# Performance work log

Measured on AMD Instinct MI355X. Metric: run time of the kernel, lower is better.

The kernel has to match this reference:

```python
import jax, jax.numpy as jnp
import numpy as np

V = 32000   # vocab_size
E = 512     # embedding_dim
H = 512     # hidden_dim
B = 16      # batch
T = 128     # max_decoder_length
S = 512     # max_encoder_length
D = 2       # directions (bidirectional encoder)


def setup_inputs() -> dict:
    key = jax.random.key(0)
    ks = jax.random.split(key, 16)
    sc = 0.02
    x = jax.random.randint(ks[0], (B, T), 0, V, dtype=jnp.int32)
    x_lengths = jax.random.randint(ks[1], (B,), 1, T + 1, dtype=jnp.int32)
    h0 = jax.random.normal(ks[2], (1, B, H), jnp.float32) * sc
    c0 = jax.random.normal(ks[3], (1, B, H), jnp.float32) * sc
    encoder_outputs = jax.random.normal(ks[4], (B, S, D * H), jnp.float32) * sc
    emb = jax.random.normal(ks[5], (V, E), jnp.float32) * sc
    emb = emb.at[0].set(0.0)  # padding_idx=0
    W_att = jax.random.normal(ks[6], (2 * H + E, S), jnp.float32) * sc
    b_att = jnp.zeros((S,), jnp.float32)
    W_ih = jax.random.normal(ks[7], (4 * H, E + H), jnp.float32) * sc
    W_hh = jax.random.normal(ks[8], (4 * H, H), jnp.float32) * sc
    b_ih = jnp.zeros((4 * H,), jnp.float32)
    b_hh = jnp.zeros((4 * H,), jnp.float32)
    W_align = jax.random.normal(ks[9], (2 * H, H), jnp.float32) * sc
    b_align = jnp.zeros((H,), jnp.float32)
    W_out = jax.random.normal(ks[10], (H, V), jnp.float32) * sc
    b_out = jnp.zeros((V,), jnp.float32)
    return dict(x=x, x_lengths=x_lengths, h0=h0, c0=c0,
                encoder_outputs=encoder_outputs, emb=emb,
                W_att=W_att, b_att=b_att,
                W_ih=W_ih, W_hh=W_hh, b_ih=b_ih, b_hh=b_hh,
                W_align=W_align, b_align=b_align,
                W_out=W_out, b_out=b_out)


def reference(x, x_lengths, h0, c0, encoder_outputs, emb, W_att, b_att,
              W_ih, W_hh, b_ih, b_hh, W_align, b_align, W_out, b_out):
    # embedding (dropout_rate=0 -> identity)
    xe = emb[x]                                       # [B,T,E]
    # context from initial state (num_layers=1)
    context = (h0 + c0).reshape(B, 1, H)              # view(B, L, H), L=1
    context = jnp.sum(context, axis=1, keepdims=True) # [B,1,H]
    context = jnp.broadcast_to(context, (B, T, H))
    lstm_input = jnp.concatenate([context, xe], axis=-1)  # [B,T,H+E]

    # single-layer LSTM over time with packed-sequence semantics:
    # state frozen and output zeroed for t >= length
    def step(carry, inp):
        h, c = carry
        x_t, t = inp                                   # x_t: [B,H+E]
        gates = x_t @ W_ih.T + h @ W_hh.T + b_ih + b_hh
        i, f, g, o = jnp.split(gates, 4, axis=-1)
        i = jax.nn.sigmoid(i); f = jax.nn.sigmoid(f)
        g = jnp.tanh(g);       o = jax.nn.sigmoid(o)
        c_new = f * c + i * g
        h_new = o * jnp.tanh(c_new)
        valid = (t < x_lengths)[:, None]
        h2 = jnp.where(valid, h_new, h)
        c2 = jnp.where(valid, c_new, c)
        return (h2, c2), jnp.where(valid, h_new, 0.0)

    ts = jnp.arange(T)
    (_, _), outs = jax.lax.scan(step, (h0[0], c0[0]),
                                (jnp.swapaxes(lstm_input, 0, 1), ts))
    lstm_output = jnp.swapaxes(outs, 0, 1)            # [B,T,H]

    # encoder_outputs: view(dir, B, S, H) then sum over directions
    enc = encoder_outputs.reshape(D, B, S, H).sum(0)  # [B,S,H]

    attention_input = jnp.concatenate([lstm_output, lstm_input], axis=-1)  # [B,T,2H+E]
    att_logits = jax.lax.stop_gradient(attention_input @ W_att + b_att)    # no_grad in torch
    soft = jax.nn.softmax(att_logits, axis=-1)        # [B,T,S]
    h_t_bar = jnp.einsum('bts,bsh->bth', soft, enc)   # [B,T,H]

    # attention targets: 0 at t=0, (S//T)*t otherwise
    tgt_row = (S // T) * jnp.arange(T, dtype=jnp.int32)
    tgt_row = tgt_row.at[0].set(0)
    attention_targets = jnp.broadcast_to(tgt_row, (B, T))

    aligned = jax.nn.sigmoid(
        jnp.concatenate([lstm_output, h_t_bar], axis=-1) @ W_align + b_align)
    out = lstm_output + h_t_bar * aligned
    out = out @ W_out + b_out                          # [B,T,V]
    return (out, jax.lax.stop_gradient(attention_input), attention_targets)
```

## Files before the change

kernel.cpp:

```cpp
#include <hip/hip_runtime.h>
#include <hip/hip_bf16.h>
#include <math.h>


typedef __attribute__((ext_vector_type(8))) short short8;
typedef __attribute__((ext_vector_type(4))) float floatx4;
typedef __attribute__((ext_vector_type(4))) int intx4;
typedef __hip_bfloat16 bf16;

__device__ __forceinline__ float b2f(bf16 v){ return __bfloat162float(v); }
__device__ __forceinline__ bf16 f2b(float v){ return __float2bfloat16(v); }
__device__ __forceinline__ float ld(const void* p, long i, int f32){
  return f32 ? ((const float*)p)[i] : b2f(((const bf16*)p)[i]);
}

__global__ void k_detect(const unsigned short* __restrict__ h0u, int* __restrict__ flags){
  if (threadIdx.x == 0){
    int bad = 0;
    for (int i=0;i<256;i++){
      int e = (h0u[i] >> 7) & 0xFF;
      if (e != 0 && (e < 100 || e > 140)) bad++;
    }
    flags[0] = (bad > 32) ? 1 : 0;
    flags[1] = 0;
  }
}

__global__ void k_prep(const int* __restrict__ x, const void* __restrict__ h0,
                       const void* __restrict__ c0, const void* __restrict__ emb,
                       const int* __restrict__ flags, bf16* __restrict__ lstm_input,
                       bf16* __restrict__ att_ws, float* __restrict__ state0,
                       bf16* __restrict__ hbuf){
  int f32 = flags[0];
  int idx = blockIdx.x*256 + threadIdx.x;
  int m = idx >> 10, c = idx & 1023;
  float v;
  if (c < 512){
    int b = m >> 7;
    v = ld(h0, b*512 + c, f32) + ld(c0, b*512 + c, f32);
  } else {
    v = ld(emb, (long)x[m]*512 + (c - 512), f32);
  }
  bf16 bv = f2b(v);
  lstm_input[idx] = bv;
  att_ws[(long)m*1536 + 512 + c] = bv;
  if (idx < 8192){
    float hv = ld(h0, idx, f32), cv = ld(c0, idx, f32);
    hbuf[idx] = f2b(hv);
    state0[idx] = hv;
    state0[8192 + idx] = cv;
  }
}

__global__ void k_encT(const void* __restrict__ eo, const int* __restrict__ flags,
                       bf16* __restrict__ encT){
  __shared__ float tile[32][33];
  int f32 = flags[0];
  int b = blockIdx.z;
  int s0 = blockIdx.x*32, h0 = blockIdx.y*32;
  int tx = threadIdx.x, ty = threadIdx.y;
  #pragma unroll
  for (int j=0;j<4;j++){
    int s = s0 + ty + j*8;
    long o = (long)b*262144 + (long)s*512 + h0 + tx;
    tile[ty + j*8][tx] = ld(eo, o, f32) + ld(eo, 4194304 + o, f32);
  }
  __syncthreads();
  #pragma unroll
  for (int j=0;j<4;j++){
    int h = h0 + ty + j*8;
    encT[((long)b*512 + h)*512 + s0 + tx] = f2b(tile[tx][ty + j*8]);
  }
}

__global__ void k_tr(const void* __restrict__ in, bf16* __restrict__ out,
                     int R, int C, const int* __restrict__ flags){
  __shared__ float tile[32][33];
  int f32 = flags[0];
  int c0 = blockIdx.x*32, r0 = blockIdx.y*32;
  int tx = threadIdx.x, ty = threadIdx.y;
  #pragma unroll
  for (int j=0;j<4;j++)
    tile[ty+j*8][tx] = ld(in, (long)(r0+ty+j*8)*C + c0+tx, f32);
  __syncthreads();
  #pragma unroll
  for (int j=0;j<4;j++)
    out[(long)(c0+ty+j*8)*R + r0+tx] = f2b(tile[tx][ty+j*8]);
}

__global__ void k_cvtW(const void* __restrict__ w, const int* __restrict__ flags,
                       bf16* __restrict__ out, long n){
  int f32 = flags[0];
  long i = (long)blockIdx.x*256 + threadIdx.x;
  if (i < n) out[i] = f2b(ld(w, i, f32));
}

__global__ void k_cvt(const void* bih, const void* bhh, const void* batt,
                      const void* balign, const void* bout,
                      const int* __restrict__ flags, bf16* __restrict__ bb){
  int f32 = flags[0];
  int i = blockIdx.x*256 + threadIdx.x;
  if (i < 2048)      bb[i] = f2b(ld(bih, i, f32));
  else if (i < 4096) bb[i] = f2b(ld(bhh, i-2048, f32));
  else if (i < 4608) bb[i] = f2b(ld(batt, i-4096, f32));
  else if (i < 5120) bb[i] = f2b(ld(balign, i-4608, f32));
  else if (i < 37120) bb[i] = f2b(ld(bout, i-5120, f32));
}

__global__ void k_wswz(const void* __restrict__ whh, const int* __restrict__ flags,
                       bf16* __restrict__ wsw){
  int f32 = flags[0];
  int bid = blockIdx.x;
  int l = threadIdx.x;
  int p = bid >> 7, tt = (bid >> 4) & 7, ks = bid & 15;
  int g = tt >> 1, hh = tt & 1;
  int row = g*512 + p*32 + hh*16 + (l & 15);
  int k = ks*32 + (l >> 4)*8;
  #pragma unroll
  for (int j=0;j<8;j++)
    wsw[(long)(bid*64 + l)*8 + j] = f2b(ld(whh, (long)row*512 + k + j, f32));
}

#define M_GX    0
#define M_F32   1
#define M_BF16  2
#define M_ALIGN 3
#define M_OUT   4

template<int MODE>
__global__ void __launch_bounds__(256)
k_gemm(const bf16* __restrict__ A, const bf16* __restrict__ Bm, int K,
       float* __restrict__ outF, bf16* __restrict__ outBH, void* __restrict__ outO,
       int ldc, const bf16* __restrict__ bias1, const bf16* __restrict__ bias2,
       const bf16* __restrict__ alin, bf16* __restrict__ finin,
       const int* __restrict__ flags, long aZ, long bZ, long cZ){
  __shared__ __align__(16) bf16 As[128*32];
  __shared__ __align__(16) bf16 Bs[128*32];
  int dfl = 0;
  if constexpr (MODE == M_OUT) dfl = flags[0];
  int tid = threadIdx.x;
  int w = tid >> 6, l = tid & 63;
  int bm = blockIdx.x, bn = blockIdx.y, bz = blockIdx.z;
  const bf16* Ag = A + bz*aZ + (long)(bm*128 + (tid>>2))*K + (tid&3)*8;
  const bf16* Bg = Bm + bz*bZ + (long)(bn*128 + (tid>>2))*K + (tid&3)*8;
  int m0 = (w&1)*64, n0 = (w>>1)*64;
  floatx4 acc[4][4];
  #pragma unroll
  for (int i=0;i<4;i++)
    #pragma unroll
    for (int j=0;j<4;j++){ floatx4 z = {0.f,0.f,0.f,0.f}; acc[i][j] = z; }

  for (int k0=0; k0<K; k0+=32){
    short8 a0 = *(const short8*)(Ag + k0);
    short8 a1 = *(const short8*)(Ag + (long)64*K + k0);
    short8 b0 = *(const short8*)(Bg + k0);
    short8 b1 = *(const short8*)(Bg + (long)64*K + k0);
    __syncthreads();
    *(short8*)(As + tid*8)        = a0;
    *(short8*)(As + 2048 + tid*8) = a1;
    *(short8*)(Bs + tid*8)        = b0;
    *(short8*)(Bs + 2048 + tid*8) = b1;
    __syncthreads();
    short8 af[4], bfr[4];
    #pragma unroll
    for (int i=0;i<4;i++){
      af[i]  = *(const short8*)(As + (m0 + i*16 + (l&15))*32 + (l>>4)*8);
      bfr[i] = *(const short8*)(Bs + (n0 + i*16 + (l&15))*32 + (l>>4)*8);
    }
    #pragma unroll
    for (int i=0;i<4;i++)
      #pragma unroll
      for (int j=0;j<4;j++)
        acc[i][j] = __builtin_amdgcn_mfma_f32_16x16x32_bf16(af[i], bfr[j], acc[i][j], 0,0,0);
  }

  int rbase = (l>>4)*4;
  int cl = l & 15;
  #pragma unroll
  for (int i=0;i<4;i++){
    #pragma unroll
    for (int j=0;j<4;j++){
      int col = bn*128 + n0 + j*16 + cl;
      #pragma unroll
      for (int r=0;r<4;r++){
        int row = bm*128 + m0 + i*16 + rbase + r;
        float v = acc[i][j][r];
        if constexpr (MODE == M_GX){
          v += b2f(bias1[col]) + b2f(bias2[col]);
          int t = row & 127, b = row >> 7;
          outF[(long)(t*16 + b)*2048 + col] = v;
        } else if constexpr (MODE == M_F32){
          v += b2f(bias1[col]);
          outF[(long)row*ldc + col] = v;
        } else if constexpr (MODE == M_BF16){
          outBH[bz*cZ + (long)row*ldc + col] = f2b(v);
        } else if constexpr (MODE == M_ALIGN){
          v += b2f(bias1[col]);
          float sg = 1.0f/(1.0f + __expf(-v));
          float lo = b2f(alin[(long)row*1024 + col]);
          float hb = b2f(alin[(long)row*1024 + 512 + col]);
          finin[(long)row*512 + col] = f2b(lo + hb*sg);
        } else {
          v += b2f(bias1[col]);
          if (dfl) ((float*)outO)[(long)row*ldc + col] = v;
          else     ((bf16*)outO)[(long)row*ldc + col] = f2b(v);
        }
      }
    }
  }
}

__global__ void k_softmax(const float* __restrict__ lg, bf16* __restrict__ soft){
  __shared__ float red[256];
  int r = blockIdx.x;
  int tid = threadIdx.x;
  float x0 = lg[(long)r*512 + tid], x1 = lg[(long)r*512 + 256 + tid];
  red[tid] = fmaxf(x0, x1); __syncthreads();
  for (int s=128; s>0; s>>=1){ if (tid<s) red[tid] = fmaxf(red[tid], red[tid+s]); __syncthreads(); }
  float mx = red[0]; __syncthreads();
  float e0 = __expf(x0-mx), e1 = __expf(x1-mx);
  red[tid] = e0+e1; __syncthreads();
  for (int s=128; s>0; s>>=1){ if (tid<s) red[tid] += red[tid+s]; __syncthreads(); }
  float inv = 1.0f/red[0];
  soft[(long)r*512 + tid] = f2b(e0*inv);
  soft[(long)r*512 + 256 + tid] = f2b(e1*inv);
}

__global__ void __launch_bounds__(256, 1)
k_lstm(const float* __restrict__ gxT, const bf16* __restrict__ wsw,
       const int* __restrict__ xlen, const float* __restrict__ state0,
       bf16* __restrict__ hbuf, int* __restrict__ flags,
       bf16* __restrict__ att_ws, bf16* __restrict__ align_in){
  int* bar = flags + 1;
  int p = blockIdx.x;
  int tid = threadIdx.x;
  int w = tid >> 6, l = tid & 63;
  __shared__ float gx_sh[16*128];
  __shared__ __align__(16) bf16 hsh[16*32];
  __shared__ int lens[16];
  if (tid < 16) lens[tid] = xlen[tid];

  short8 wfrag[2][16];
  #pragma unroll
  for (int hh=0; hh<2; hh++)
    #pragma unroll
    for (int ks=0; ks<16; ks++)
      wfrag[hh][ks] = ((const short8*)wsw)[((p*8 + (w*2+hh))*16 + ks)*64 + l];

  int b0i = tid >> 5, u = tid & 31;
  int b1i = b0i + 8;
  float h_r0 = state0[b0i*512 + p*32 + u];
  float c_r0 = state0[8192 + b0i*512 + p*32 + u];
  float h_r1 = state0[b1i*512 + p*32 + u];
  float c_r1 = state0[8192 + b1i*512 + p*32 + u];

  float gr[8];
  #pragma unroll
  for (int rep=0;rep<8;rep++){
    int idx = rep*256 + tid;
    int b = idx >> 7, jl = idx & 127;
    gr[rep] = gxT[(long)b*2048 + (jl>>5)*512 + p*32 + (jl&31)];
  }

  __syncthreads();

  for (int t=0; t<128; t++){
    #pragma unroll
    for (int rep=0;rep<8;rep++)
      gx_sh[rep*256 + tid] = gr[rep];
    if (t < 127){
      #pragma unroll
      for (int rep=0;rep<8;rep++){
        int idx = rep*256 + tid;
        int b = idx >> 7, jl = idx & 127;
        gr[rep] = gxT[(long)((t+1)*16 + b)*2048 + (jl>>5)*512 + p*32 + (jl&31)];
      }
    }
    const bf16* hb = hbuf + (long)t*8192;
    floatx4 acc0 = {0.f,0.f,0.f,0.f};
    floatx4 acc1 = {0.f,0.f,0.f,0.f};
    #pragma unroll
    for (int ks=0; ks<16; ks++){
      short8 afr = *(const short8*)(hb + (l&15)*512 + ks*32 + (l>>4)*8);
      acc0 = __builtin_amdgcn_mfma_f32_16x16x32_bf16(afr, wfrag[0][ks], acc0, 0,0,0);
      acc1 = __builtin_amdgcn_mfma_f32_16x16x32_bf16(afr, wfrag[1][ks], acc1, 0,0,0);
    }
    __syncthreads();
    #pragma unroll
    for (int r=0; r<4; r++){
      int bb = (l>>4)*4 + r;
      gx_sh[bb*128 + w*32 + (l&15)]      += acc0[r];
      gx_sh[bb*128 + w*32 + 16 + (l&15)] += acc1[r];
    }
    __syncthreads();
    {
      float ig = gx_sh[b0i*128 + u],      fg = gx_sh[b0i*128 + 32 + u];
      float gg = gx_sh[b0i*128 + 64 + u], og = gx_sh[b0i*128 + 96 + u];
      bool valid = (t < lens[b0i]);
      float ii = 1.f/(1.f+__expf(-ig)), ff = 1.f/(1.f+__expf(-fg));
      float g2 = tanhf(gg),             oo = 1.f/(1.f+__expf(-og));
      float cn = ff*c_r0 + ii*g2;
      float hn = oo*tanhf(cn);
      if (valid){ c_r0 = cn; h_r0 = hn; }
      float hout = valid ? hn : 0.0f;
      hsh[b0i*32 + u] = f2b(h_r0);
      int row = b0i*128 + t;
      att_ws[(long)row*1536 + p*32 + u]   = f2b(hout);
      align_in[(long)row*1024 + p*32 + u] = f2b(hout);
    }
    {
      float ig = gx_sh[b1i*128 + u],      fg = gx_sh[b1i*128 + 32 + u];
      float gg = gx_sh[b1i*128 + 64 + u], og = gx_sh[b1i*128 + 96 + u];
      bool valid = (t < lens[b1i]);
      float ii = 1.f/(1.f+__expf(-ig)), ff = 1.f/(1.f+__expf(-fg));
      float g2 = tanhf(gg),             oo = 1.f/(1.f+__expf(-og));
      float cn = ff*c_r1 + ii*g2;
      float hn = oo*tanhf(cn);
      if (valid){ c_r1 = cn; h_r1 = hn; }
      float hout = valid ? hn : 0.0f;
      hsh[b1i*32 + u] = f2b(h_r1);
      int row = b1i*128 + t;
      att_ws[(long)row*1536 + p*32 + u]   = f2b(hout);
      align_in[(long)row*1024 + p*32 + u] = f2b(hout);
    }
    __syncthreads();
    if (t < 127){
      if (tid < 64){
        int b = tid >> 2, ch = tid & 3;
        intx4 hv = *(const intx4*)(hsh + b*32 + ch*8);
        bf16* dst = hbuf + (long)(t+1)*8192 + b*512 + p*32 + ch*8;
        asm volatile("global_store_dwordx4 %0, %1, off sc0 sc1" :: "v"(dst), "v"(hv) : "memory");
        asm volatile("s_waitcnt vmcnt(0)" ::: "memory");
        if (tid == 0){
          __hip_atomic_fetch_add(bar, 1, __ATOMIC_RELAXED, __HIP_MEMORY_SCOPE_AGENT);
          int target = (t+1)*16;
          while (__hip_atomic_load(bar, __ATOMIC_RELAXED, __HIP_MEMORY_SCOPE_AGENT) < target)
            __builtin_amdgcn_s_sleep(1);
        }
      }
      __syncthreads();
      asm volatile("" ::: "memory");
    }
  }
}

__global__ void k_finout(const bf16* __restrict__ att_ws, const int* __restrict__ flags,
                         void* __restrict__ d_out){
  int f32 = flags[0];
  long i = (long)blockIdx.x*256 + threadIdx.x;
  if (i < 3145728){
    if (f32) ((float*)d_out)[65536000 + i] = b2f(att_ws[i]);
    else     ((bf16*)d_out)[65536000 + i] = att_ws[i];
  } else if (i < 3147776){
    long j = i - 3145728;
    float tv = (float)(4*((int)j & 127));
    if (f32) ((float*)d_out)[68681728 + j] = tv;
    else     ((bf16*)d_out)[68681728 + j] = f2b(tv);
  }
}

extern "C" void kernel_launch(void* const* d_in, const int* in_sizes, int n_in,
                              void* d_out, int out_size, void* d_ws, size_t ws_size,
                              hipStream_t stream){
  const int*  x      = (const int*) d_in[0];
  const int*  xlen   = (const int*) d_in[1];
  const void* h0     = d_in[2];
  const void* c0     = d_in[3];
  const void* eo     = d_in[4];
  const void* emb    = d_in[5];
  const void* W_att  = d_in[6];
  const void* b_att  = d_in[7];
  const void* W_ih   = d_in[8];
  const void* W_hh   = d_in[9];
  const void* b_ih   = d_in[10];
  const void* b_hh   = d_in[11];
  const void* W_align= d_in[12];
  const void* b_align= d_in[13];
  const void* W_out  = d_in[14];
  const void* b_out  = d_in[15];

  char* ws = (char*)d_ws;
  bf16*  lstm_input = (bf16*)(ws + 0);
  bf16*  encT       = (bf16*)(ws + 4194304);
  bf16*  WattT      = (bf16*)(ws + 12582912);
  bf16*  WalignT    = (bf16*)(ws + 14155776);
  bf16*  WoutT      = (bf16*)(ws + 15204352);
  bf16*  Wsw        = (bf16*)(ws + 47972352);
  float* gxT        = (float*)(ws + 50069504);
  float* attlog     = (float*)(ws + 66846720);
  bf16*  soft       = (bf16*)(ws + 71041024);
  bf16*  align_in   = (bf16*)(ws + 73138176);
  bf16*  final_in   = (bf16*)(ws + 77332480);
  bf16*  hbuf       = (bf16*)(ws + 77332480);
  bf16*  att_ws     = (bf16*)(ws + 79429632);
  bf16*  bb         = (bf16*)(ws + 85721088);
  float* state0     = (float*)(ws + 85795328);
  bf16*  WihB       = (bf16*)(ws + 85893632);
  int*   flags      = (int*) (ws + 90087936);

  k_detect<<<1, 64, 0, stream>>>((const unsigned short*)h0, flags);
  k_prep<<<8192, 256, 0, stream>>>(x, h0, c0, emb, flags, lstm_input, att_ws, state0, hbuf);
  k_cvt<<<146, 256, 0, stream>>>(b_ih, b_hh, b_att, b_align, b_out, flags, bb);
  k_cvtW<<<8192, 256, 0, stream>>>(W_ih, flags, WihB, 2097152L);
  k_encT<<<dim3(16,16,16), dim3(32,8), 0, stream>>>(eo, flags, encT);
  k_tr<<<dim3(16,48),  dim3(32,8), 0, stream>>>(W_att,   WattT,   1536, 512, flags);
  k_tr<<<dim3(16,32),  dim3(32,8), 0, stream>>>(W_align, WalignT, 1024, 512, flags);
  k_tr<<<dim3(1000,16),dim3(32,8), 0, stream>>>(W_out,   WoutT,   512, 32000, flags);
  k_wswz<<<2048, 64, 0, stream>>>(W_hh, flags, Wsw);

  k_gemm<M_GX><<<dim3(16,16,1), 256, 0, stream>>>(lstm_input, WihB, 1024,
      gxT, nullptr, nullptr, 0, bb, bb+2048, nullptr, nullptr, flags, 0, 0, 0);

  k_lstm<<<16, 256, 0, stream>>>(gxT, Wsw, xlen, state0, hbuf, flags, att_ws, align_in);

  k_gemm<M_F32><<<dim3(16,4,1), 256, 0, stream>>>(att_ws, WattT, 1536,
      attlog, nullptr, nullptr, 512, bb+4096, nullptr, nullptr, nullptr, flags, 0, 0, 0);

  k_softmax<<<2048, 256, 0, stream>>>(attlog, soft);

  k_gemm<M_BF16><<<dim3(1,4,16), 256, 0, stream>>>(soft, encT, 512,
      nullptr, align_in + 512, nullptr, 1024, nullptr, nullptr, nullptr, nullptr,
      flags, 65536L, 262144L, 131072L);

  k_gemm<M_ALIGN><<<dim3(16,4,1), 256, 0, stream>>>(align_in, WalignT, 1024,
      nullptr, nullptr, nullptr, 0, bb+4608, nullptr, align_in, final_in, flags, 0, 0, 0);

  k_gemm<M_OUT><<<dim3(16,250,1), 256, 0, stream>>>(final_in, WoutT, 512,
      nullptr, nullptr, d_out, 32000, bb+5120, nullptr, nullptr, nullptr, flags, 0, 0, 0);

  k_finout<<<12296, 256, 0, stream>>>(att_ws, flags, d_out);
}
```

Measured before the change: 1.273 ms.

## Replace LSTM grid barrier with sentinel-polled h buffer; stage W_hh in LDS

```diff
diff --git a/kernel.cpp b/kernel.cpp
--- a/kernel.cpp
+++ b/kernel.cpp
@@ -12,6 +12,15 @@
 __device__ __forceinline__ bf16 f2b(float v){ return __float2bfloat16(v); }
 __device__ __forceinline__ float ld(const void* p, long i, int f32){
   return f32 ? ((const float*)p)[i] : b2f(((const bf16*)p)[i]);
+}
+
+#define SENTI ((int)0xFFC1FFC1u)
+
+__device__ __forceinline__ intx4 poll16(const void* pp){
+  intx4 r;
+  asm volatile("global_load_dwordx4 %0, %1, off sc0 sc1\n\ts_waitcnt vmcnt(0)"
+               : "=v"(r) : "v"(pp) : "memory");
+  return r;
 }
 
 __global__ void k_detect(const unsigned short* __restrict__ h0u, int* __restrict__ flags){
@@ -22,7 +31,6 @@
       if (e != 0 && (e < 100 || e > 140)) bad++;
     }
     flags[0] = (bad > 32) ? 1 : 0;
-    flags[1] = 0;
   }
 }
 
@@ -50,6 +58,11 @@
     state0[idx] = hv;
     state0[8192 + idx] = cv;
   }
+}
+
+__global__ void k_sent(int* __restrict__ hbuf32){
+  long i = (long)blockIdx.x*256 + threadIdx.x;
+  if (i < 520192) hbuf32[4096 + i] = SENTI;
 }
 
 __global__ void k_encT(const void* __restrict__ eo, const int* __restrict__ flags,
@@ -231,21 +244,20 @@
        const int* __restrict__ xlen, const float* __restrict__ state0,
        bf16* __restrict__ hbuf, int* __restrict__ flags,
        bf16* __restrict__ att_ws, bf16* __restrict__ align_in){
-  int* bar = flags + 1;
   int p = blockIdx.x;
   int tid = threadIdx.x;
-  int w = tid >> 6, l = tid & 63;
+  int w = tid >> 6, l = tid & 63, w2 = w*2;
+  __shared__ __align__(16) short8 wlds[8192];
   __shared__ float gx_sh[16*128];
   __shared__ __align__(16) bf16 hsh[16*32];
   __shared__ int lens[16];
   if (tid < 16) lens[tid] = xlen[tid];
 
-  short8 wfrag[2][16];
-  #pragma unroll
-  for (int hh=0; hh<2; hh++)
-    #pragma unroll
-    for (int ks=0; ks<16; ks++)
-      wfrag[hh][ks] = ((const short8*)wsw)[((p*8 + (w*2+hh))*16 + ks)*64 + l];
+  {
+    const short8* wsrc = (const short8*)wsw + (long)p*8192;
+    #pragma unroll
+    for (int i=0;i<32;i++) wlds[i*256 + tid] = wsrc[i*256 + tid];
+  }
 
   int b0i = tid >> 5, u = tid & 31;
   int b1i = b0i + 8;
@@ -268,6 +280,40 @@
     #pragma unroll
     for (int rep=0;rep<8;rep++)
       gx_sh[rep*256 + tid] = gr[rep];
+
+    const char* hbp = (const char*)hbuf + (long)t*16384 + ((l&15)*1024 + (l>>4)*16);
+    intx4 a0,a1,a2,a3,a4,a5,a6,a7,a8,a9,a10,a11,a12,a13,a14,a15;
+    asm volatile(
+      "global_load_dwordx4 %0,  %16, off sc0 sc1\n\t"
+      "global_load_dwordx4 %1,  %16, off offset:64  sc0 sc1\n\t"
+      "global_load_dwordx4 %2,  %16, off offset:128 sc0 sc1\n\t"
+      "global_load_dwordx4 %3,  %16, off offset:192 sc0 sc1\n\t"
+      "global_load_dwordx4 %4,  %16, off offset:256 sc0 sc1\n\t"
+      "global_load_dwordx4 %5,  %16, off offset:320 sc0 sc1\n\t"
+      "global_load_dwordx4 %6,  %16, off offset:384 sc0 sc1\n\t"
+      "global_load_dwordx4 %7,  %16, off offset:448 sc0 sc1\n\t"
+      "global_load_dwordx4 %8,  %16, off offset:512 sc0 sc1\n\t"
+      "global_load_dwordx4 %9,  %16, off offset:576 sc0 sc1\n\t"
+      "global_load_dwordx4 %10, %16, off offset:640 sc0 sc1\n\t"
+      "global_load_dwordx4 %11, %16, off offset:704 sc0 sc1\n\t"
+      "global_load_dwordx4 %12, %16, off offset:768 sc0 sc1\n\t"
+      "global_load_dwordx4 %13, %16, off offset:832 sc0 sc1\n\t"
+      "global_load_dwordx4 %14, %16, off offset:896 sc0 sc1\n\t"
+      "global_load_dwordx4 %15, %16, off offset:960 sc0 sc1\n\t"
+      "s_waitcnt vmcnt(0)"
+      : "=v"(a0),"=v"(a1),"=v"(a2),"=v"(a3),"=v"(a4),"=v"(a5),"=v"(a6),"=v"(a7),
+        "=v"(a8),"=v"(a9),"=v"(a10),"=v"(a11),"=v"(a12),"=v"(a13),"=v"(a14),"=v"(a15)
+      : "v"(hbp)
+      : "memory");
+    #define RETRY(A, OFF) \
+      while (__builtin_expect(A.x==SENTI || A.y==SENTI || A.z==SENTI || A.w==SENTI, 0)) \
+        A = poll16(hbp + (OFF));
+    RETRY(a0,0)    RETRY(a1,64)   RETRY(a2,128)  RETRY(a3,192)
+    RETRY(a4,256)  RETRY(a5,320)  RETRY(a6,384)  RETRY(a7,448)
+    RETRY(a8,512)  RETRY(a9,576)  RETRY(a10,640) RETRY(a11,704)
+    RETRY(a12,768) RETRY(a13,832) RETRY(a14,896) RETRY(a15,960)
+    #undef RETRY
+
     if (t < 127){
       #pragma unroll
       for (int rep=0;rep<8;rep++){
@@ -276,16 +322,20 @@
         gr[rep] = gxT[(long)((t+1)*16 + b)*2048 + (jl>>5)*512 + p*32 + (jl&31)];
       }
     }
-    const bf16* hb = hbuf + (long)t*8192;
+
     floatx4 acc0 = {0.f,0.f,0.f,0.f};
     floatx4 acc1 = {0.f,0.f,0.f,0.f};
-    #pragma unroll
-    for (int ks=0; ks<16; ks++){
-      short8 afr = *(const short8*)(hb + (l&15)*512 + ks*32 + (l>>4)*8);
-      acc0 = __builtin_amdgcn_mfma_f32_16x16x32_bf16(afr, wfrag[0][ks], acc0, 0,0,0);
-      acc1 = __builtin_amdgcn_mfma_f32_16x16x32_bf16(afr, wfrag[1][ks], acc1, 0,0,0);
-    }
+    #define STEPK(K, AK) { \
+      short8 av = __builtin_bit_cast(short8, AK); \
+      acc0 = __builtin_amdgcn_mfma_f32_16x16x32_bf16(av, wlds[(w2*16+(K))*64 + l], acc0, 0,0,0); \
+      acc1 = __builtin_amdgcn_mfma_f32_16x16x32_bf16(av, wlds[((w2+1)*16+(K))*64 + l], acc1, 0,0,0); }
+    STEPK(0,a0)   STEPK(1,a1)   STEPK(2,a2)   STEPK(3,a3)
+    STEPK(4,a4)   STEPK(5,a5)   STEPK(6,a6)   STEPK(7,a7)
+    STEPK(8,a8)   STEPK(9,a9)   STEPK(10,a10) STEPK(11,a11)
+    STEPK(12,a12) STEPK(13,a13) STEPK(14,a14) STEPK(15,a15)
+    #undef STEPK
     __syncthreads();
+
     #pragma unroll
     for (int r=0; r<4; r++){
       int bb = (l>>4)*4 + r;
@@ -293,6 +343,7 @@
       gx_sh[bb*128 + w*32 + 16 + (l&15)] += acc1[r];
     }
     __syncthreads();
+
     {
       float ig = gx_sh[b0i*128 + u],      fg = gx_sh[b0i*128 + 32 + u];
       float gg = gx_sh[b0i*128 + 64 + u], og = gx_sh[b0i*128 + 96 + u];
@@ -324,22 +375,12 @@
       align_in[(long)row*1024 + p*32 + u] = f2b(hout);
     }
     __syncthreads();
-    if (t < 127){
-      if (tid < 64){
-        int b = tid >> 2, ch = tid & 3;
-        intx4 hv = *(const intx4*)(hsh + b*32 + ch*8);
-        bf16* dst = hbuf + (long)(t+1)*8192 + b*512 + p*32 + ch*8;
-        asm volatile("global_store_dwordx4 %0, %1, off sc0 sc1" :: "v"(dst), "v"(hv) : "memory");
-        asm volatile("s_waitcnt vmcnt(0)" ::: "memory");
-        if (tid == 0){
-          __hip_atomic_fetch_add(bar, 1, __ATOMIC_RELAXED, __HIP_MEMORY_SCOPE_AGENT);
-          int target = (t+1)*16;
-          while (__hip_atomic_load(bar, __ATOMIC_RELAXED, __HIP_MEMORY_SCOPE_AGENT) < target)
-            __builtin_amdgcn_s_sleep(1);
-        }
-      }
-      __syncthreads();
-      asm volatile("" ::: "memory");
+
+    if (t < 127 && tid < 64){
+      int b = tid >> 2, ch = tid & 3;
+      intx4 hv = *(const intx4*)(hsh + b*32 + ch*8);
+      bf16* dst = hbuf + (long)(t+1)*8192 + b*512 + p*32 + ch*8;
+      asm volatile("global_store_dwordx4 %0, %1, off sc0 sc1" :: "v"(dst), "v"(hv) : "memory");
     }
   }
 }
@@ -400,6 +441,7 @@
 
   k_detect<<<1, 64, 0, stream>>>((const unsigned short*)h0, flags);
   k_prep<<<8192, 256, 0, stream>>>(x, h0, c0, emb, flags, lstm_input, att_ws, state0, hbuf);
+  k_sent<<<2032, 256, 0, stream>>>((int*)hbuf);
   k_cvt<<<146, 256, 0, stream>>>(b_ih, b_hh, b_att, b_align, b_out, flags, bb);
   k_cvtW<<<8192, 256, 0, stream>>>(W_ih, flags, WihB, 2097152L);
   k_encT<<<dim3(16,16,16), dim3(32,8), 0, stream>>>(eo, flags, encT);
```

Result: no change. 1.296 ms (+1.8%).
